# Optimization experiments

Hardware: AMD Instinct MI355X
Metric: run time of the kernel (lower is better)

Reference implementation:

```python
import jax, jax.numpy as jnp
import numpy as np

NUM_NODES = 2   # number of iResNet blocks
H = 256         # internal_size
L = 4           # num_internal_layers (hidden Linear+ELU layers)
D = 2           # inp_size_linear (2D uv coords)
N = 1048576     # number of points (flattened 1024x1024 STMap grid)


def setup_inputs() -> dict:
    key = jax.random.key(0)
    ks = jax.random.split(key, 7)
    scale = 0.8 / np.sqrt(H)  # mimic lipschitz_correction (spectral norm <= 0.8)
    uv = jax.random.normal(ks[0], (N, D), jnp.float32)
    w_in = jax.random.normal(ks[1], (NUM_NODES, D, H), jnp.float32) * (0.8 / np.sqrt(D))
    b_in = jax.random.normal(ks[2], (NUM_NODES, H), jnp.float32) * 0.01
    w_hid = jax.random.normal(ks[3], (NUM_NODES, L, H, H), jnp.float32) * scale
    b_hid = jax.random.normal(ks[4], (NUM_NODES, L, H), jnp.float32) * 0.01
    w_out = jax.random.normal(ks[5], (NUM_NODES, H, D), jnp.float32) * scale
    b_out = jax.random.normal(ks[6], (NUM_NODES, D), jnp.float32) * 0.01
    return {"uv": uv, "w_in": w_in, "b_in": b_in, "w_hid": w_hid,
            "b_hid": b_hid, "w_out": w_out, "b_out": b_out}


def reference(uv, w_in, b_in, w_hid, b_hid, w_out, b_out):
    # Chain of NUM_NODES invertible ResNet blocks (forward / sensor_to_frustum):
    #   x <- x + MLP(x),  MLP = Lin(D,H)+ELU, L x (Lin(H,H)+ELU), Lin(H,D)
    x = uv  # [N, D]
    for i in range(NUM_NODES):
        h = jax.nn.elu(x @ w_in[i] + b_in[i])          # [N, H]
        for l in range(L):
            h = jax.nn.elu(h @ w_hid[i, l] + b_hid[i, l])
        x = x + (h @ w_out[i] + b_out[i])              # residual add, [N, D]
    return x
```

## Files before the change

### kernel.cpp

```cpp
#include <hip/hip_runtime.h>
#include <stdint.h>

typedef short bf16x8 __attribute__((ext_vector_type(8)));
typedef float f32x16 __attribute__((ext_vector_type(16)));
typedef float f32x4  __attribute__((ext_vector_type(4)));
typedef float f32x2  __attribute__((ext_vector_type(2)));

#define NODES  2
#define LAYERS 4
#define HD     256
#define MTILE  128
#define QBYTES 32768
#define NQ     (NODES*LAYERS*4)

__device__ __forceinline__ unsigned short f2bf(float f) {
  unsigned u = __float_as_uint(f);
  u += 0x7fffu + ((u >> 16) & 1u);
  return (unsigned short)(u >> 16);
}
__device__ __forceinline__ float bf2f(unsigned short s) {
  return __uint_as_float(((unsigned)s) << 16);
}
__device__ __forceinline__ float elu1(float v) {
  return v > 0.0f ? v : (__expf(v) - 1.0f);
}
__device__ __forceinline__ unsigned cvtpk(float lo, float hi) {
  unsigned r;
  asm("v_cvt_pk_bf16_f32 %0, %1, %2" : "=v"(r) : "v"(lo), "v"(hi));
  return r;
}
union U8 { bf16x8 v; unsigned u[4]; };

#define GLOAD_LDS16(gsrc, ldst)                                                        \
  __builtin_amdgcn_global_load_lds(                                                    \
      (const __attribute__((address_space(1))) unsigned int*)(gsrc),                   \
      (__attribute__((address_space(3))) unsigned int*)(ldst), 16, 0, 0)

__global__ __launch_bounds__(256) void convw_kernel(const float* __restrict__ w_hid,
                                                    unsigned short* __restrict__ blob) {
  int e = blockIdx.x * 256 + threadIdx.x;
  int nl = e >> 16;
  int k  = (e >> 8) & 255;
  int n  = e & 255;
  float v = w_hid[(nl * 256 + k) * 256 + n];
  int qq    = k >> 6;
  int c_loc = (k >> 4) & 3;
  int k16   = k & 15;
  int g     = (k16 >> 2) & 1;
  int i     = (k16 & 3) + ((k16 >> 3) << 2);
  int pos   = (c_loc << 4) + (g << 3) + i;
  unsigned boff = ((unsigned)(nl * 4 + qq) << 15)
                + ((unsigned)n << 7)
                + (((unsigned)(pos << 1)) ^ ((unsigned)((n & 7) << 4)));
  blob[boff >> 1] = f2bf(v);
}

__global__ __launch_bounds__(256, 2) void nld_kernel(
    const float* __restrict__ uv, const float* __restrict__ w_in,
    const float* __restrict__ b_in, const float* __restrict__ b_hid,
    const float* __restrict__ w_out, const float* __restrict__ b_out,
    const unsigned short* __restrict__ blob, float* __restrict__ out, int nrows) {

  __shared__ __attribute__((aligned(16))) char  w_sm[2][QBYTES];
  __shared__ __attribute__((aligned(16))) float pb_hid[NODES * LAYERS * HD];
  __shared__ __attribute__((aligned(16))) float pb_in[NODES * HD];

  const int t    = threadIdx.x;
  const int lane = t & 63;
  const int wv   = t >> 6;
  const int l31  = lane & 31;
  const int g    = lane >> 5;
  const long row = (long)blockIdx.x * MTILE + wv * 32 + l31;

  auto stage = [&](int i) {
    const char* src = (const char*)blob + (size_t)i * QBYTES + t * 16;
    char* dst = &w_sm[i & 1][t * 16];
#pragma unroll
    for (int r = 0; r < 8; ++r) GLOAD_LDS16(src + r * 4096, dst + r * 4096);
  };

  stage(0);
  for (int i = t; i < NODES * LAYERS * HD; i += 256) pb_hid[i] = b_hid[i];
  for (int i = t; i < NODES * HD; i += 256) pb_in[i] = b_in[i];

  float x0 = 0.0f, x1 = 0.0f;
  if (row < nrows) { f32x2 u = *(const f32x2*)(uv + row * 2); x0 = u[0]; x1 = u[1]; }
  __syncthreads();

  bf16x8 hb[16];
  const unsigned swz = (unsigned)((l31 & 7) << 4);
  const unsigned rowb = (unsigned)(l31 * 128);

  for (int nd = 0; nd < NODES; ++nd) {
    {
      const float* wi0 = w_in + nd * 2 * HD;
      const float* wi1 = wi0 + HD;
      const float* bi  = &pb_in[nd * HD];
#pragma unroll
      for (int c = 0; c < 16; ++c) {
        int kb = 16 * c + 4 * g;
        f32x4 a0 = *(const f32x4*)(wi0 + kb);
        f32x4 a1 = *(const f32x4*)(wi0 + kb + 8);
        f32x4 c0 = *(const f32x4*)(wi1 + kb);
        f32x4 c1 = *(const f32x4*)(wi1 + kb + 8);
        f32x4 e0 = *(const f32x4*)(bi + kb);
        f32x4 e1 = *(const f32x4*)(bi + kb + 8);
        float v0 = elu1(fmaf(x1, c0[0], fmaf(x0, a0[0], e0[0])));
        float v1 = elu1(fmaf(x1, c0[1], fmaf(x0, a0[1], e0[1])));
        float v2 = elu1(fmaf(x1, c0[2], fmaf(x0, a0[2], e0[2])));
        float v3 = elu1(fmaf(x1, c0[3], fmaf(x0, a0[3], e0[3])));
        float v4 = elu1(fmaf(x1, c1[0], fmaf(x0, a1[0], e1[0])));
        float v5 = elu1(fmaf(x1, c1[1], fmaf(x0, a1[1], e1[1])));
        float v6 = elu1(fmaf(x1, c1[2], fmaf(x0, a1[2], e1[2])));
        float v7 = elu1(fmaf(x1, c1[3], fmaf(x0, a1[3], e1[3])));
        U8 p;
        p.u[0] = cvtpk(v0, v1); p.u[1] = cvtpk(v2, v3);
        p.u[2] = cvtpk(v4, v5); p.u[3] = cvtpk(v6, v7);
        hb[c] = p.v;
      }
    }

    for (int ly = 0; ly < LAYERS; ++ly) {
      f32x16 acc[8];
#pragma unroll
      for (int nf = 0; nf < 8; ++nf)
#pragma unroll
        for (int j = 0; j < 16; ++j) acc[nf][j] = 0.0f;

      const int iq0 = (nd * LAYERS + ly) * 4;
#pragma unroll
      for (int qq = 0; qq < 4; ++qq) {
        int iq = iq0 + qq;
        __syncthreads();
        if (iq + 1 < NQ) stage(iq + 1);
        const char* wbuf = &w_sm[iq & 1][0];
        __builtin_amdgcn_s_setprio(1);
#pragma unroll
        for (int kc = 0; kc < 4; ++kc) {
          unsigned koff = (unsigned)(32 * kc + 16 * g) ^ swz;
#pragma unroll
          for (int nf = 0; nf < 8; ++nf) {
            bf16x8 wf = *(const bf16x8*)(wbuf + 4096 * nf + rowb + koff);
            acc[nf] = __builtin_amdgcn_mfma_f32_32x32x16_bf16(wf, hb[4 * qq + kc],
                                                              acc[nf], 0, 0, 0);
          }
        }
        __builtin_amdgcn_s_setprio(0);
      }

      const float* bl = &pb_hid[(nd * LAYERS + ly) * HD];
#pragma unroll
      for (int nf = 0; nf < 8; ++nf) {
        int nb = 32 * nf + 4 * g;
        f32x4 b0 = *(const f32x4*)(bl + nb);
        f32x4 b1 = *(const f32x4*)(bl + nb + 8);
        f32x4 b2 = *(const f32x4*)(bl + nb + 16);
        f32x4 b3 = *(const f32x4*)(bl + nb + 24);
        float e[16];
#pragma unroll
        for (int j = 0; j < 4; ++j) {
          e[j]      = elu1(acc[nf][j]      + b0[j]);
          e[4 + j]  = elu1(acc[nf][4 + j]  + b1[j]);
          e[8 + j]  = elu1(acc[nf][8 + j]  + b2[j]);
          e[12 + j] = elu1(acc[nf][12 + j] + b3[j]);
        }
        U8 p, q;
        p.u[0] = cvtpk(e[0],  e[1]);  p.u[1] = cvtpk(e[2],  e[3]);
        p.u[2] = cvtpk(e[4],  e[5]);  p.u[3] = cvtpk(e[6],  e[7]);
        q.u[0] = cvtpk(e[8],  e[9]);  q.u[1] = cvtpk(e[10], e[11]);
        q.u[2] = cvtpk(e[12], e[13]); q.u[3] = cvtpk(e[14], e[15]);
        hb[2 * nf]     = p.v;
        hb[2 * nf + 1] = q.v;
      }
    }

    {
      const float* wo = w_out + nd * HD * 2;
      float s0 = 0.0f, s1 = 0.0f;
#pragma unroll
      for (int c = 0; c < 16; ++c) {
        int kb = 16 * c + 4 * g;
        f32x4 wA0 = *(const f32x4*)(wo + kb * 2);
        f32x4 wA1 = *(const f32x4*)(wo + kb * 2 + 4);
        f32x4 wB0 = *(const f32x4*)(wo + (kb + 8) * 2);
        f32x4 wB1 = *(const f32x4*)(wo + (kb + 8) * 2 + 4);
        bf16x8 hv = hb[c];
        float f0 = bf2f((unsigned short)hv[0]), f1 = bf2f((unsigned short)hv[1]);
        float f2 = bf2f((unsigned short)hv[2]), f3 = bf2f((unsigned short)hv[3]);
        float f4 = bf2f((unsigned short)hv[4]), f5 = bf2f((unsigned short)hv[5]);
        float f6 = bf2f((unsigned short)hv[6]), f7 = bf2f((unsigned short)hv[7]);
        s0 = fmaf(f0, wA0[0], s0); s1 = fmaf(f0, wA0[1], s1);
        s0 = fmaf(f1, wA0[2], s0); s1 = fmaf(f1, wA0[3], s1);
        s0 = fmaf(f2, wA1[0], s0); s1 = fmaf(f2, wA1[1], s1);
        s0 = fmaf(f3, wA1[2], s0); s1 = fmaf(f3, wA1[3], s1);
        s0 = fmaf(f4, wB0[0], s0); s1 = fmaf(f4, wB0[1], s1);
        s0 = fmaf(f5, wB0[2], s0); s1 = fmaf(f5, wB0[3], s1);
        s0 = fmaf(f6, wB1[0], s0); s1 = fmaf(f6, wB1[1], s1);
        s0 = fmaf(f7, wB1[2], s0); s1 = fmaf(f7, wB1[3], s1);
      }
      s0 += __shfl_xor(s0, 32);
      s1 += __shfl_xor(s1, 32);
      x0 += s0 + b_out[nd * 2 + 0];
      x1 += s1 + b_out[nd * 2 + 1];
    }
  }

  if (row < nrows && g == 0) {
    f32x2 r; r[0] = x0; r[1] = x1;
    *(f32x2*)(out + row * 2) = r;
  }
}

extern "C" void kernel_launch(void* const* d_in, const int* in_sizes, int n_in,
                              void* d_out, int out_size, void* d_ws, size_t ws_size,
                              hipStream_t stream) {
  const float* uv    = (const float*)d_in[0];
  const float* w_in  = (const float*)d_in[1];
  const float* b_in  = (const float*)d_in[2];
  const float* w_hid = (const float*)d_in[3];
  const float* b_hid = (const float*)d_in[4];
  const float* w_out = (const float*)d_in[5];
  const float* b_out = (const float*)d_in[6];
  unsigned short* blob = (unsigned short*)d_ws;

  int whid_elems = in_sizes[3];
  convw_kernel<<<whid_elems / 256, 256, 0, stream>>>(w_hid, blob);

  int N = in_sizes[0] / 2;
  int grid = (N + MTILE - 1) / MTILE;
  nld_kernel<<<grid, 256, 0, stream>>>(uv, w_in, b_in, b_hid, w_out, b_out,
                                       blob, (float*)d_out, N);
}
```

Measured before the change: 1.290 ms.

## Repack weight blob into fragment-contiguous layout and seed accumulators with bias

Changes the bf16 weight blob layout so each lane's MFMA A-fragment sits at a linear offset (kc, g, nf, lane), replacing the XOR-swizzled row layout. Weight LDS reads then become contiguous 16-byte loads with immediate offsets, which removes per-read address math and should avoid bank conflicts. Accumulators are now initialised with the bias instead of zero, so the separate bias add in the epilogue goes away. This relies on the converter and the reader agreeing exactly on the new layout.

```diff
diff --git a/kernel.cpp b/kernel.cpp
--- a/kernel.cpp
+++ b/kernel.cpp
@@ -43,15 +43,15 @@
   int k  = (e >> 8) & 255;
   int n  = e & 255;
   float v = w_hid[(nl * 256 + k) * 256 + n];
-  int qq    = k >> 6;
-  int c_loc = (k >> 4) & 3;
-  int k16   = k & 15;
-  int g     = (k16 >> 2) & 1;
-  int i     = (k16 & 3) + ((k16 >> 3) << 2);
-  int pos   = (c_loc << 4) + (g << 3) + i;
+  int qq  = k >> 6;
+  int kc  = (k >> 4) & 3;
+  int k16 = k & 15;
+  int g   = (k16 >> 2) & 1;
+  int i   = (k16 & 3) | ((k16 >> 3) << 2);
+  int nf  = n >> 5, l31 = n & 31;
   unsigned boff = ((unsigned)(nl * 4 + qq) << 15)
-                + ((unsigned)n << 7)
-                + (((unsigned)(pos << 1)) ^ ((unsigned)((n & 7) << 4)));
+                + ((unsigned)kc << 13) + ((unsigned)g << 12)
+                + ((unsigned)nf << 9) + ((unsigned)l31 << 4) + ((unsigned)i << 1);
   blob[boff >> 1] = f2bf(v);
 }
 
@@ -88,8 +88,9 @@
   __syncthreads();
 
   bf16x8 hb[16];
-  const unsigned swz = (unsigned)((l31 & 7) << 4);
-  const unsigned rowb = (unsigned)(l31 * 128);
+  const unsigned fbase = (unsigned)(g * 4096 + l31 * 16);
+  const char* wq0 = &w_sm[0][0];
+  const char* wq1 = &w_sm[1][0];
 
   for (int nd = 0; nd < NODES; ++nd) {
     {
@@ -121,34 +122,8 @@
     }
 
     for (int ly = 0; ly < LAYERS; ++ly) {
+      const float* bl = &pb_hid[(nd * LAYERS + ly) * HD];
       f32x16 acc[8];
-#pragma unroll
-      for (int nf = 0; nf < 8; ++nf)
-#pragma unroll
-        for (int j = 0; j < 16; ++j) acc[nf][j] = 0.0f;
-
-      const int iq0 = (nd * LAYERS + ly) * 4;
-#pragma unroll
-      for (int qq = 0; qq < 4; ++qq) {
-        int iq = iq0 + qq;
-        __syncthreads();
-        if (iq + 1 < NQ) stage(iq + 1);
-        const char* wbuf = &w_sm[iq & 1][0];
-        __builtin_amdgcn_s_setprio(1);
-#pragma unroll
-        for (int kc = 0; kc < 4; ++kc) {
-          unsigned koff = (unsigned)(32 * kc + 16 * g) ^ swz;
-#pragma unroll
-          for (int nf = 0; nf < 8; ++nf) {
-            bf16x8 wf = *(const bf16x8*)(wbuf + 4096 * nf + rowb + koff);
-            acc[nf] = __builtin_amdgcn_mfma_f32_32x32x16_bf16(wf, hb[4 * qq + kc],
-                                                              acc[nf], 0, 0, 0);
-          }
-        }
-        __builtin_amdgcn_s_setprio(0);
-      }
-
-      const float* bl = &pb_hid[(nd * LAYERS + ly) * HD];
 #pragma unroll
       for (int nf = 0; nf < 8; ++nf) {
         int nb = 32 * nf + 4 * g;
@@ -156,14 +131,40 @@
         f32x4 b1 = *(const f32x4*)(bl + nb + 8);
         f32x4 b2 = *(const f32x4*)(bl + nb + 16);
         f32x4 b3 = *(const f32x4*)(bl + nb + 24);
+#pragma unroll
+        for (int j = 0; j < 4; ++j) {
+          acc[nf][j]      = b0[j];
+          acc[nf][4 + j]  = b1[j];
+          acc[nf][8 + j]  = b2[j];
+          acc[nf][12 + j] = b3[j];
+        }
+      }
+
+      const int iq0 = (nd * LAYERS + ly) * 4;
+#pragma unroll
+      for (int qq = 0; qq < 4; ++qq) {
+        int iq = iq0 + qq;
+        __syncthreads();
+        if (iq + 1 < NQ) stage(iq + 1);
+        const char* wbuf = ((iq & 1) ? wq1 : wq0) + fbase;
+        __builtin_amdgcn_s_setprio(1);
+#pragma unroll
+        for (int kc = 0; kc < 4; ++kc) {
+#pragma unroll
+          for (int nf = 0; nf < 8; ++nf) {
+            bf16x8 wf = *(const bf16x8*)(wbuf + kc * 8192 + nf * 512);
+            acc[nf] = __builtin_amdgcn_mfma_f32_32x32x16_bf16(wf, hb[4 * qq + kc],
+                                                              acc[nf], 0, 0, 0);
+          }
+        }
+        __builtin_amdgcn_s_setprio(0);
+      }
+
+#pragma unroll
+      for (int nf = 0; nf < 8; ++nf) {
         float e[16];
 #pragma unroll
-        for (int j = 0; j < 4; ++j) {
-          e[j]      = elu1(acc[nf][j]      + b0[j]);
-          e[4 + j]  = elu1(acc[nf][4 + j]  + b1[j]);
-          e[8 + j]  = elu1(acc[nf][8 + j]  + b2[j]);
-          e[12 + j] = elu1(acc[nf][12 + j] + b3[j]);
-        }
+        for (int j = 0; j < 16; ++j) e[j] = elu1(acc[nf][j]);
         U8 p, q;
         p.u[0] = cvtpk(e[0],  e[1]);  p.u[1] = cvtpk(e[2],  e[3]);
         p.u[2] = cvtpk(e[4],  e[5]);  p.u[3] = cvtpk(e[6],  e[7]);
```

Result: faster. 1.246 ms (-3.4%).
